# Kernel optimization log

Hardware: AMD Instinct MI355X
Metric: run time of the kernel (lower is better)

Reference implementation:

```python
import jax, jax.numpy as jnp
import numpy as np

W_IMG, H_IMG = 800.0, 600.0          # BoxList.size (w, h)
BBOX_W = (10.0, 10.0, 5.0, 5.0)      # BoxCoder weights
BBOX_CLAMP = float(np.log(1000.0 / 16.0))
SCORE_THRESH = 0.05
NMS_THRESH = 0.5
TOPN_PER_CLS = 300
DET_PER_IMG = 100


def setup_inputs() -> dict:
    key = jax.random.key(0)
    kl, kb, kp, kf = jax.random.split(key, 4)
    B, N, C, D = 2, 512, 151, 4096
    # spread logits so softmax produces scores above the 0.05 threshold
    class_logits = jax.random.normal(kl, (B, N, C), jnp.float32) * 4.0
    box_regression = jax.random.normal(kb, (B, N, C * 4), jnp.float32) * 0.2
    # valid xyxy proposal boxes inside the image
    pts = jax.random.uniform(kp, (B, N, 2, 2), jnp.float32)
    pts = pts * jnp.array([W_IMG - 1.0, H_IMG - 1.0], jnp.float32)
    lo = jnp.min(pts, axis=2)
    hi = jnp.max(pts, axis=2)
    proposal_boxes = jnp.concatenate([lo, hi], axis=-1)
    features = jax.random.normal(kf, (B, N, D), jnp.float32)
    return {"class_logits": class_logits, "box_regression": box_regression,
            "proposal_boxes": proposal_boxes, "features": features}


def decode_boxes(reg, boxes):
    wx, wy, ww, wh = BBOX_W
    widths = boxes[..., 2] - boxes[..., 0] + 1.0
    heights = boxes[..., 3] - boxes[..., 1] + 1.0
    ctr_x = boxes[..., 0] + 0.5 * widths
    ctr_y = boxes[..., 1] + 0.5 * heights
    dx = reg[..., 0] / wx
    dy = reg[..., 1] / wy
    dw = jnp.minimum(reg[..., 2] / ww, BBOX_CLAMP)
    dh = jnp.minimum(reg[..., 3] / wh, BBOX_CLAMP)
    pcx = dx * widths[..., None] + ctr_x[..., None]
    pcy = dy * heights[..., None] + ctr_y[..., None]
    pw = jnp.exp(dw) * widths[..., None]
    ph = jnp.exp(dh) * heights[..., None]
    return jnp.stack([pcx - 0.5 * pw, pcy - 0.5 * ph,
                      pcx + 0.5 * pw - 1.0, pcy + 0.5 * ph - 1.0], axis=-1)


def pairwise_iou(b):
    area = (b[:, 2] - b[:, 0] + 1.0) * (b[:, 3] - b[:, 1] + 1.0)
    xx1 = jnp.maximum(b[:, None, 0], b[None, :, 0])
    yy1 = jnp.maximum(b[:, None, 1], b[None, :, 1])
    xx2 = jnp.minimum(b[:, None, 2], b[None, :, 2])
    yy2 = jnp.minimum(b[:, None, 3], b[None, :, 3])
    inter = jnp.maximum(xx2 - xx1 + 1.0, 0.0) * jnp.maximum(yy2 - yy1 + 1.0, 0.0)
    return inter / (area[:, None] + area[None, :] - inter)


def class_nms(boxes, scores, valid):
    # Greedy NMS over one class of one image; fixed-shape, returns keep mask in
    # the ORIGINAL proposal order. `valid` = score > SCORE_THRESH prefilter.
    N = scores.shape[0]
    order = jnp.argsort(-scores)
    b = jax.lax.stop_gradient(boxes[order])
    v = valid[order]
    iou = pairwise_iou(b)
    idx = jnp.arange(N)
    def body(i, keep):
        sup = (iou[i] > NMS_THRESH) & (idx > i) & keep[i]
        return keep & ~sup
    keep = jax.lax.fori_loop(0, N, body, v)
    keep = keep & (jnp.cumsum(keep) <= TOPN_PER_CLS)  # post-NMS per-class top-n
    return jnp.zeros(N, bool).at[order].set(keep)


def reference(class_logits, box_regression, proposal_boxes, features):
    B, N, C = class_logits.shape
    prob = jax.nn.softmax(class_logits, axis=-1)                 # [B,N,C]
    reg = box_regression.reshape(B, N, C, 4)
    boxes = decode_boxes(reg, proposal_boxes)                    # [B,N,C,4]
    # clip_to_image(remove_empty=False)
    x = jnp.clip(boxes[..., 0::2], 0.0, W_IMG - 1.0)
    y = jnp.clip(boxes[..., 1::2], 0.0, H_IMG - 1.0)
    boxes = jnp.stack([x[..., 0], y[..., 0], x[..., 1], y[..., 1]], axis=-1)
    valid = prob > SCORE_THRESH                                  # [B,N,C]
    # per-(image, class) NMS, vectorized via vmap
    boxes_c = jnp.swapaxes(boxes, 1, 2)                          # [B,C,N,4]
    scores_c = jnp.swapaxes(prob, 1, 2)                          # [B,C,N]
    valid_c = jnp.swapaxes(valid, 1, 2)
    keep_c = jax.vmap(jax.vmap(class_nms))(boxes_c, scores_c, valid_c)
    keep = jnp.swapaxes(keep_c, 1, 2)                            # [B,N,C]
    keep = keep & (jnp.arange(C)[None, None, :] != 0)            # drop background
    # nms_filter_duplicates: one (score, label) per proposal
    dist_scores = prob * keep
    labels = jnp.argmax(dist_scores, axis=-1)                    # [B,N]
    scores_pre = jnp.max(dist_scores, axis=-1)                   # [B,N]
    det_valid = scores_pre > 0
    # detections_per_img cap via kth-largest threshold (only if over the cap)
    num = jnp.sum(det_valid, axis=-1)                            # [B]
    kth = jax.lax.top_k(jnp.where(det_valid, scores_pre, -1.0), DET_PER_IMG)[0][:, -1]
    thr = jnp.where(num > DET_PER_IMG, kth, -1.0)
    det_valid = det_valid & (scores_pre >= thr[:, None])
    # gather box of the winning class: boxes_per_cls[final_inds, labels_pre]
    final_boxes = jnp.take_along_axis(boxes, labels[..., None, None], axis=2)[:, :, 0, :]
    final_boxes = jnp.where(det_valid[..., None], final_boxes, 0.0)
    final_scores = jnp.where(det_valid, scores_pre, 0.0)
    final_labels = jnp.where(det_valid, labels, 0)
    nms_features = features * det_valid[..., None]               # features[orig_inds]
    return final_boxes, final_scores, final_labels, det_valid, nms_features
```

## Files before the change

### kernel.cpp

```cpp
#include <hip/hip_runtime.h>
#include <math.h>

#define Bn 2
#define Nn 512
#define Cn 151
#define Dn 4096
#define W_IMG 800.0f
#define H_IMG 600.0f
#define SCORE_T 0.05f
#define NMS_T 0.5f
#define TOPN 300
#define DETMAX 100
#define BBOX_CLAMP 4.135166556742356f

#define OFF_BOXES  ((size_t)0)
#define OFF_SCORES ((size_t)(Bn * Nn * 4))
#define OFF_LABELS (OFF_SCORES + (size_t)(Bn * Nn))
#define OFF_VALID  (OFF_LABELS + (size_t)(Bn * Nn))
#define OFF_FEATS  (OFF_VALID + (size_t)(Bn * Nn))

__global__ void kA_softmax_decode(const float* __restrict__ logits,
                                  const float* __restrict__ reg,
                                  const float* __restrict__ props,
                                  float* __restrict__ prob_t,
                                  float* __restrict__ boxes,
                                  unsigned long long* __restrict__ packed) {
  const int wave = threadIdx.x >> 6;
  const int lane = threadIdx.x & 63;
  const int bn = blockIdx.x * 4 + wave;
  const int b = bn >> 9;
  const int n = bn & (Nn - 1);

  const float* lrow = logits + (size_t)bn * Cn;
  const float l0 = lrow[lane];
  const float l1 = lrow[lane + 64];
  const float l2 = (lane + 128 < Cn) ? lrow[lane + 128] : -INFINITY;

  float mx = fmaxf(l0, fmaxf(l1, l2));
  #pragma unroll
  for (int o = 32; o > 0; o >>= 1) mx = fmaxf(mx, __shfl_xor(mx, o));

  const float e0 = expf(l0 - mx);
  const float e1 = expf(l1 - mx);
  const float e2 = (lane + 128 < Cn) ? expf(l2 - mx) : 0.0f;
  float sum = e0 + e1 + e2;
  #pragma unroll
  for (int o = 32; o > 0; o >>= 1) sum += __shfl_xor(sum, o);
  const float inv = 1.0f / sum;

  float* pt = prob_t + (size_t)b * Cn * Nn + n;
  pt[(size_t)lane * Nn] = e0 * inv;
  pt[(size_t)(lane + 64) * Nn] = e1 * inv;
  if (lane + 128 < Cn) pt[(size_t)(lane + 128) * Nn] = e2 * inv;

  const float bx1 = props[bn * 4 + 0];
  const float by1 = props[bn * 4 + 1];
  const float bx2 = props[bn * 4 + 2];
  const float by2 = props[bn * 4 + 3];
  const float w = bx2 - bx1 + 1.0f;
  const float h = by2 - by1 + 1.0f;
  const float cx = bx1 + 0.5f * w;
  const float cy = by1 + 0.5f * h;

  #pragma unroll
  for (int rr = 0; rr < 3; ++rr) {
    const int c = lane + rr * 64;
    if (c < Cn) {
      const float* r = reg + ((size_t)bn * Cn + c) * 4;
      const float dx = r[0] * 0.1f;
      const float dy = r[1] * 0.1f;
      const float dw = fminf(r[2] * 0.2f, BBOX_CLAMP);
      const float dh = fminf(r[3] * 0.2f, BBOX_CLAMP);
      const float pcx = dx * w + cx;
      const float pcy = dy * h + cy;
      const float pw = expf(dw) * w;
      const float ph = expf(dh) * h;
      float x1 = pcx - 0.5f * pw;
      float y1 = pcy - 0.5f * ph;
      float x2 = pcx + 0.5f * pw - 1.0f;
      float y2 = pcy + 0.5f * ph - 1.0f;
      x1 = fminf(fmaxf(x1, 0.0f), W_IMG - 1.0f);
      x2 = fminf(fmaxf(x2, 0.0f), W_IMG - 1.0f);
      y1 = fminf(fmaxf(y1, 0.0f), H_IMG - 1.0f);
      y2 = fminf(fmaxf(y2, 0.0f), H_IMG - 1.0f);
      float* ob = boxes + ((size_t)bn * Cn + c) * 4;
      ob[0] = x1; ob[1] = y1; ob[2] = x2; ob[3] = y2;
    }
  }

  if (lane == 0) packed[bn] = 0ull;
}

__global__ void kB_nms(const float* __restrict__ prob_t,
                       const float* __restrict__ boxes,
                       unsigned long long* __restrict__ packed) {
  const int bc = blockIdx.x;
  const int b = bc / Cn;
  const int c = bc % Cn;
  const int lane = threadIdx.x;
  if (c == 0) return;

  __shared__ float ls[Nn];
  __shared__ int   ln[Nn];
  __shared__ float ss2[64];
  __shared__ int   sn2[64];
  __shared__ float fs[Nn];
  __shared__ int   fn[Nn];
  __shared__ float fb[Nn][4];
  __shared__ unsigned char kp[Nn];

  const float* col = prob_t + ((size_t)b * Cn + c) * Nn;
  int base = 0;
  #pragma unroll
  for (int j = 0; j < Nn / 64; ++j) {
    const int n = j * 64 + lane;
    const float s = col[n];
    const bool v = s > SCORE_T;
    const unsigned long long m = __ballot(v);
    if (v) {
      const int pos = base + __popcll(m & ((1ull << lane) - 1ull));
      ls[pos] = s; ln[pos] = n;
    }
    base += __popcll(m);
  }
  const int M = base;
  if (M == 0) return;
  __syncthreads();

  if (M <= 64) {
    float s = -1.0f; int n = -1;
    if (lane < M) { s = ls[lane]; n = ln[lane]; }
    int rank = 0;
    for (int j = 0; j < M; ++j) {
      const float sj = __shfl(s, j);
      const int nj = __shfl(n, j);
      if (lane < M) rank += (sj > s) || (sj == s && nj < n);
    }
    if (lane < M) { ss2[rank] = s; sn2[rank] = n; }
    __syncthreads();

    float sc = 0.0f; int sn = 0;
    float x1 = 0.0f, y1 = 0.0f, x2 = 0.0f, y2 = 0.0f;
    if (lane < M) {
      sc = ss2[lane]; sn = sn2[lane];
      const float4 bp = *(const float4*)(boxes + (((size_t)b * Nn + sn) * Cn + c) * 4);
      x1 = bp.x; y1 = bp.y; x2 = bp.z; y2 = bp.w;
    }
    const float area = (x2 - x1 + 1.0f) * (y2 - y1 + 1.0f);

    unsigned long long live = (M >= 64) ? ~0ull : ((1ull << M) - 1ull);
    int i = 0;
    while (i < 64) {
      const unsigned long long rem = live & (~0ull << i);
      if (!rem) break;
      i = __ffsll(rem) - 1;
      const float ax1 = __shfl(x1, i), ay1 = __shfl(y1, i);
      const float ax2 = __shfl(x2, i), ay2 = __shfl(y2, i);
      const float aarea = (ax2 - ax1 + 1.0f) * (ay2 - ay1 + 1.0f);
      const float xx1 = fmaxf(ax1, x1), yy1 = fmaxf(ay1, y1);
      const float xx2 = fminf(ax2, x2), yy2 = fminf(ay2, y2);
      const float inter = fmaxf(xx2 - xx1 + 1.0f, 0.0f) * fmaxf(yy2 - yy1 + 1.0f, 0.0f);
      const float iou = inter / (aarea + area - inter);
      const bool sup = (lane > i) && (lane < M) && ((live >> lane) & 1ull) && (iou > NMS_T);
      live &= ~__ballot(sup);
      ++i;
    }
    if (lane < M && ((live >> lane) & 1ull)) {
      const unsigned long long key =
          ((unsigned long long)__float_as_uint(sc) << 32) | (unsigned int)(Cn - c);
      atomicMax(&packed[(size_t)b * Nn + sn], key);
    }
  } else {
    for (int i0 = lane; i0 < M; i0 += 64) {
      const float si = ls[i0]; const int ni = ln[i0];
      int r = 0;
      for (int j = 0; j < M; ++j) {
        const float sj = ls[j]; const int nj = ln[j];
        r += (sj > si) || (sj == si && nj < ni);
      }
      fs[r] = si; fn[r] = ni;
    }
    __syncthreads();
    for (int i0 = lane; i0 < M; i0 += 64) {
      const float4 bp = *(const float4*)(boxes + (((size_t)b * Nn + fn[i0]) * Cn + c) * 4);
      fb[i0][0] = bp.x; fb[i0][1] = bp.y; fb[i0][2] = bp.z; fb[i0][3] = bp.w;
      kp[i0] = 1;
    }
    __syncthreads();
    for (int i = 0; i < M; ++i) {
      if (!kp[i]) continue;
      const float ax1 = fb[i][0], ay1 = fb[i][1], ax2 = fb[i][2], ay2 = fb[i][3];
      const float aarea = (ax2 - ax1 + 1.0f) * (ay2 - ay1 + 1.0f);
      for (int t = i + 1 + lane; t < M; t += 64) {
        if (kp[t]) {
          const float bx1 = fb[t][0], by1 = fb[t][1], bx2 = fb[t][2], by2 = fb[t][3];
          const float barea = (bx2 - bx1 + 1.0f) * (by2 - by1 + 1.0f);
          const float xx1 = fmaxf(ax1, bx1), yy1 = fmaxf(ay1, by1);
          const float xx2 = fminf(ax2, bx2), yy2 = fminf(ay2, by2);
          const float inter = fmaxf(xx2 - xx1 + 1.0f, 0.0f) * fmaxf(yy2 - yy1 + 1.0f, 0.0f);
          if (inter / (aarea + barea - inter) > NMS_T) kp[t] = 0;
        }
      }
      __syncthreads();
    }
    if (lane == 0) {
      int cnt = 0;
      for (int t = 0; t < M; ++t)
        if (kp[t]) { if (++cnt > TOPN) kp[t] = 0; }
    }
    __syncthreads();
    for (int t = lane; t < M; t += 64) {
      if (kp[t]) {
        const unsigned long long key =
            ((unsigned long long)__float_as_uint(fs[t]) << 32) | (unsigned int)(Cn - c);
        atomicMax(&packed[(size_t)b * Nn + fn[t]], key);
      }
    }
  }
}

__global__ void kC_final(const unsigned long long* __restrict__ packed,
                         const float* __restrict__ boxes,
                         float* __restrict__ out) {
  const int b = blockIdx.x;
  const int n = threadIdx.x;
  __shared__ float v[Nn];
  __shared__ int wcnt[8];
  __shared__ float sThr;

  const unsigned long long p = packed[(size_t)b * Nn + n];
  const float s = __uint_as_float((unsigned int)(p >> 32));
  const int label = (p != 0ull) ? (Cn - (int)(p & 0xFFFFFFFFull)) : 0;
  const bool pos = (s > 0.0f);
  v[n] = pos ? s : -1.0f;

  const unsigned long long bal = __ballot(pos);
  if ((n & 63) == 0) wcnt[n >> 6] = __popcll(bal);
  __syncthreads();
  int num = 0;
  #pragma unroll
  for (int i = 0; i < 8; ++i) num += wcnt[i];

  for (int k = 2; k <= Nn; k <<= 1) {
    for (int j = k >> 1; j > 0; j >>= 1) {
      const int ixj = n ^ j;
      if (ixj > n) {
        const bool up = ((n & k) == 0);
        const float a = v[n], bb = v[ixj];
        if (up != (a > bb) && a != bb) { v[n] = bb; v[ixj] = a; }
      }
      __syncthreads();
    }
  }
  if (n == 0) sThr = (num > DETMAX) ? v[DETMAX - 1] : -1.0f;
  __syncthreads();

  const bool valid = pos && (s >= sThr);
  const int i = b * Nn + n;
  float4 ob = make_float4(0.0f, 0.0f, 0.0f, 0.0f);
  if (valid) ob = *(const float4*)(boxes + (((size_t)i) * Cn + label) * 4);
  *(float4*)(out + OFF_BOXES + (size_t)i * 4) = ob;
  out[OFF_SCORES + i] = valid ? s : 0.0f;
  out[OFF_LABELS + i] = valid ? (float)label : 0.0f;
  out[OFF_VALID + i] = valid ? 1.0f : 0.0f;
}

__global__ void kD_feats(const float* __restrict__ feats,
                         const float* __restrict__ valid,
                         float* __restrict__ out) {
  const int row = blockIdx.x;
  const float m = valid[row];
  const float4* fi = (const float4*)(feats + (size_t)row * Dn);
  float4* fo = (float4*)(out + (size_t)row * Dn);
  #pragma unroll 4
  for (int t = threadIdx.x; t < Dn / 4; t += 256) {
    float4 x = fi[t];
    x.x *= m; x.y *= m; x.z *= m; x.w *= m;
    fo[t] = x;
  }
}

extern "C" void kernel_launch(void* const* d_in, const int* in_sizes, int n_in,
                              void* d_out, int out_size, void* d_ws, size_t ws_size,
                              hipStream_t stream) {
  const float* logits = (const float*)d_in[0];
  const float* reg    = (const float*)d_in[1];
  const float* props  = (const float*)d_in[2];
  const float* feats  = (const float*)d_in[3];
  float* out = (float*)d_out;

  unsigned long long* packed = (unsigned long long*)d_ws;
  float* prob_t = (float*)(packed + Bn * Nn);
  float* boxes  = prob_t + (size_t)Bn * Cn * Nn;

  kA_softmax_decode<<<Bn * Nn / 4, 256, 0, stream>>>(logits, reg, props,
                                                     prob_t, boxes, packed);
  kB_nms<<<Bn * Cn, 64, 0, stream>>>(prob_t, boxes, packed);
  kC_final<<<Bn, Nn, 0, stream>>>(packed, boxes, out);
  kD_feats<<<Bn * Nn, 256, 0, stream>>>(feats, out + OFF_VALID, out + OFF_FEATS);
}
```

Baseline: 97.67 us.

## Decode boxes lazily in NMS and final kernels, skip sort when under cap

Box decoding no longer runs eagerly for every (proposal, class) pair in the softmax kernel, and the decoded boxes are no longer written to a workspace buffer. NMS and the final gather now decode on demand, only for the candidates that pass the score threshold. This removes a large write and re-read of boxes and the exp work for pairs that are never used. The final kernel also skips the bitonic sort when the detection count is at or below the cap. The cost is some recomputation, and the division by 10 and 5 in place of multiplying by 0.1 and 0.2 may change rounding slightly.

```diff
diff --git a/kernel.cpp b/kernel.cpp
--- a/kernel.cpp
+++ b/kernel.cpp
@@ -19,12 +19,33 @@
 #define OFF_VALID  (OFF_LABELS + (size_t)(Bn * Nn))
 #define OFF_FEATS  (OFF_VALID + (size_t)(Bn * Nn))
 
-__global__ void kA_softmax_decode(const float* __restrict__ logits,
-                                  const float* __restrict__ reg,
-                                  const float* __restrict__ props,
-                                  float* __restrict__ prob_t,
-                                  float* __restrict__ boxes,
-                                  unsigned long long* __restrict__ packed) {
+__device__ __forceinline__ float4 decode_clip(const float4 pr, const float4 rg) {
+  const float w = pr.z - pr.x + 1.0f;
+  const float h = pr.w - pr.y + 1.0f;
+  const float cx = pr.x + 0.5f * w;
+  const float cy = pr.y + 0.5f * h;
+  const float dx = rg.x / 10.0f;
+  const float dy = rg.y / 10.0f;
+  const float dw = fminf(rg.z / 5.0f, BBOX_CLAMP);
+  const float dh = fminf(rg.w / 5.0f, BBOX_CLAMP);
+  const float pcx = dx * w + cx;
+  const float pcy = dy * h + cy;
+  const float pw = expf(dw) * w;
+  const float ph = expf(dh) * h;
+  float x1 = pcx - 0.5f * pw;
+  float y1 = pcy - 0.5f * ph;
+  float x2 = pcx + 0.5f * pw - 1.0f;
+  float y2 = pcy + 0.5f * ph - 1.0f;
+  x1 = fminf(fmaxf(x1, 0.0f), W_IMG - 1.0f);
+  x2 = fminf(fmaxf(x2, 0.0f), W_IMG - 1.0f);
+  y1 = fminf(fmaxf(y1, 0.0f), H_IMG - 1.0f);
+  y2 = fminf(fmaxf(y2, 0.0f), H_IMG - 1.0f);
+  return make_float4(x1, y1, x2, y2);
+}
+
+__global__ void kA_softmax(const float* __restrict__ logits,
+                           float* __restrict__ prob_t,
+                           unsigned long long* __restrict__ packed) {
   const int wave = threadIdx.x >> 6;
   const int lane = threadIdx.x & 63;
   const int bn = blockIdx.x * 4 + wave;
@@ -53,46 +74,12 @@
   pt[(size_t)(lane + 64) * Nn] = e1 * inv;
   if (lane + 128 < Cn) pt[(size_t)(lane + 128) * Nn] = e2 * inv;
 
-  const float bx1 = props[bn * 4 + 0];
-  const float by1 = props[bn * 4 + 1];
-  const float bx2 = props[bn * 4 + 2];
-  const float by2 = props[bn * 4 + 3];
-  const float w = bx2 - bx1 + 1.0f;
-  const float h = by2 - by1 + 1.0f;
-  const float cx = bx1 + 0.5f * w;
-  const float cy = by1 + 0.5f * h;
-
-  #pragma unroll
-  for (int rr = 0; rr < 3; ++rr) {
-    const int c = lane + rr * 64;
-    if (c < Cn) {
-      const float* r = reg + ((size_t)bn * Cn + c) * 4;
-      const float dx = r[0] * 0.1f;
-      const float dy = r[1] * 0.1f;
-      const float dw = fminf(r[2] * 0.2f, BBOX_CLAMP);
-      const float dh = fminf(r[3] * 0.2f, BBOX_CLAMP);
-      const float pcx = dx * w + cx;
-      const float pcy = dy * h + cy;
-      const float pw = expf(dw) * w;
-      const float ph = expf(dh) * h;
-      float x1 = pcx - 0.5f * pw;
-      float y1 = pcy - 0.5f * ph;
-      float x2 = pcx + 0.5f * pw - 1.0f;
-      float y2 = pcy + 0.5f * ph - 1.0f;
-      x1 = fminf(fmaxf(x1, 0.0f), W_IMG - 1.0f);
-      x2 = fminf(fmaxf(x2, 0.0f), W_IMG - 1.0f);
-      y1 = fminf(fmaxf(y1, 0.0f), H_IMG - 1.0f);
-      y2 = fminf(fmaxf(y2, 0.0f), H_IMG - 1.0f);
-      float* ob = boxes + ((size_t)bn * Cn + c) * 4;
-      ob[0] = x1; ob[1] = y1; ob[2] = x2; ob[3] = y2;
-    }
-  }
-
   if (lane == 0) packed[bn] = 0ull;
 }
 
 __global__ void kB_nms(const float* __restrict__ prob_t,
-                       const float* __restrict__ boxes,
+                       const float* __restrict__ reg,
+                       const float* __restrict__ props,
                        unsigned long long* __restrict__ packed) {
   const int bc = blockIdx.x;
   const int b = bc / Cn;
@@ -143,8 +130,11 @@
     float x1 = 0.0f, y1 = 0.0f, x2 = 0.0f, y2 = 0.0f;
     if (lane < M) {
       sc = ss2[lane]; sn = sn2[lane];
-      const float4 bp = *(const float4*)(boxes + (((size_t)b * Nn + sn) * Cn + c) * 4);
-      x1 = bp.x; y1 = bp.y; x2 = bp.z; y2 = bp.w;
+      const int i = b * Nn + sn;
+      const float4 pr = *(const float4*)(props + (size_t)i * 4);
+      const float4 rg = *(const float4*)(reg + ((size_t)i * Cn + c) * 4);
+      const float4 bx = decode_clip(pr, rg);
+      x1 = bx.x; y1 = bx.y; x2 = bx.z; y2 = bx.w;
     }
     const float area = (x2 - x1 + 1.0f) * (y2 - y1 + 1.0f);
 
@@ -182,8 +172,11 @@
     }
     __syncthreads();
     for (int i0 = lane; i0 < M; i0 += 64) {
-      const float4 bp = *(const float4*)(boxes + (((size_t)b * Nn + fn[i0]) * Cn + c) * 4);
-      fb[i0][0] = bp.x; fb[i0][1] = bp.y; fb[i0][2] = bp.z; fb[i0][3] = bp.w;
+      const int i = b * Nn + fn[i0];
+      const float4 pr = *(const float4*)(props + (size_t)i * 4);
+      const float4 rg = *(const float4*)(reg + ((size_t)i * Cn + c) * 4);
+      const float4 bx = decode_clip(pr, rg);
+      fb[i0][0] = bx.x; fb[i0][1] = bx.y; fb[i0][2] = bx.z; fb[i0][3] = bx.w;
       kp[i0] = 1;
     }
     __syncthreads();
@@ -220,7 +213,8 @@
 }
 
 __global__ void kC_final(const unsigned long long* __restrict__ packed,
-                         const float* __restrict__ boxes,
+                         const float* __restrict__ reg,
+                         const float* __restrict__ props,
                          float* __restrict__ out) {
   const int b = blockIdx.x;
   const int n = threadIdx.x;
@@ -241,24 +235,32 @@
   #pragma unroll
   for (int i = 0; i < 8; ++i) num += wcnt[i];
 
-  for (int k = 2; k <= Nn; k <<= 1) {
-    for (int j = k >> 1; j > 0; j >>= 1) {
-      const int ixj = n ^ j;
-      if (ixj > n) {
-        const bool up = ((n & k) == 0);
-        const float a = v[n], bb = v[ixj];
-        if (up != (a > bb) && a != bb) { v[n] = bb; v[ixj] = a; }
+  if (num > DETMAX) {
+    for (int k = 2; k <= Nn; k <<= 1) {
+      for (int j = k >> 1; j > 0; j >>= 1) {
+        const int ixj = n ^ j;
+        if (ixj > n) {
+          const bool up = ((n & k) == 0);
+          const float a = v[n], bb = v[ixj];
+          if (up != (a > bb) && a != bb) { v[n] = bb; v[ixj] = a; }
+        }
+        __syncthreads();
       }
-      __syncthreads();
-    }
-  }
-  if (n == 0) sThr = (num > DETMAX) ? v[DETMAX - 1] : -1.0f;
+    }
+    if (n == 0) sThr = v[DETMAX - 1];
+  } else {
+    if (n == 0) sThr = -1.0f;
+  }
   __syncthreads();
 
   const bool valid = pos && (s >= sThr);
   const int i = b * Nn + n;
   float4 ob = make_float4(0.0f, 0.0f, 0.0f, 0.0f);
-  if (valid) ob = *(const float4*)(boxes + (((size_t)i) * Cn + label) * 4);
+  if (valid) {
+    const float4 pr = *(const float4*)(props + (size_t)i * 4);
+    const float4 rg = *(const float4*)(reg + ((size_t)i * Cn + label) * 4);
+    ob = decode_clip(pr, rg);
+  }
   *(float4*)(out + OFF_BOXES + (size_t)i * 4) = ob;
   out[OFF_SCORES + i] = valid ? s : 0.0f;
   out[OFF_LABELS + i] = valid ? (float)label : 0.0f;
@@ -291,11 +293,9 @@
 
   unsigned long long* packed = (unsigned long long*)d_ws;
   float* prob_t = (float*)(packed + Bn * Nn);
-  float* boxes  = prob_t + (size_t)Bn * Cn * Nn;
-
-  kA_softmax_decode<<<Bn * Nn / 4, 256, 0, stream>>>(logits, reg, props,
-                                                     prob_t, boxes, packed);
-  kB_nms<<<Bn * Cn, 64, 0, stream>>>(prob_t, boxes, packed);
-  kC_final<<<Bn, Nn, 0, stream>>>(packed, boxes, out);
+
+  kA_softmax<<<Bn * Nn / 4, 256, 0, stream>>>(logits, prob_t, packed);
+  kB_nms<<<Bn * Cn, 64, 0, stream>>>(prob_t, reg, props, packed);
+  kC_final<<<Bn, Nn, 0, stream>>>(packed, reg, props, out);
   kD_feats<<<Bn * Nn, 256, 0, stream>>>(feats, out + OFF_VALID, out + OFF_FEATS);
 }
```

Result: no change. 96.98 us (-0.7%).
